# Performance work log

Hardware: AMD Instinct MI355X
Metric: run time of the kernel (lower is better)

## Reference

```python
import math
import jax, jax.numpy as jnp
import numpy as np

B, T, T_P, C, H = 4, 2048, 256, 768, 12
HD = C // H


def setup_inputs() -> dict:
    key = jax.random.key(0)
    k1, k2, k3, k4 = jax.random.split(key, 4)
    x = jax.random.normal(k1, (B, T, C), dtype=jnp.float32)
    prefix = jax.random.normal(k2, (B, T_P, C), dtype=jnp.float32)
    # torch nn.Linear weight layout: (out_features, in_features)
    W_qkv = jax.random.normal(k3, (3 * C, C), dtype=jnp.float32) * (1.0 / math.sqrt(C))
    W_out = jax.random.normal(k4, (C, C), dtype=jnp.float32) * (1.0 / math.sqrt(C))
    return {"x": x, "prefix": prefix, "W_qkv": W_qkv, "W_out": W_out}


def _mac_causal_mask(t_p: int, t: int) -> jnp.ndarray:
    total = t_p + t
    mask = jnp.zeros((total, total), dtype=bool)
    mask = mask.at[:t_p, t_p:].set(True)  # h tokens blocked from x tokens
    causal = jnp.triu(jnp.ones((t, t), dtype=bool), k=1)  # causal within x block
    return mask.at[t_p:, t_p:].set(causal)


def reference(x, prefix, W_qkv, W_out):
    b, t, c = x.shape
    t_p = prefix.shape[1]
    t_all = t_p + t
    x_full = jnp.concatenate([prefix, x], axis=1)          # (B, T_all, C)
    qkv = x_full @ W_qkv.T                                  # (B, T_all, 3C)
    q, k, v = jnp.split(qkv, 3, axis=-1)
    # (B, H, T_all, HD)
    q = q.reshape(b, t_all, H, HD).transpose(0, 2, 1, 3)
    k = k.reshape(b, t_all, H, HD).transpose(0, 2, 1, 3)
    v = v.reshape(b, t_all, H, HD).transpose(0, 2, 1, 3)
    scale = 1.0 / math.sqrt(HD)
    att = jnp.einsum('bhqd,bhkd->bhqk', q, k) * scale       # (B, H, T_all, T_all)
    mask = _mac_causal_mask(t_p, t)
    att = jnp.where(mask[None, None], -jnp.inf, att)
    att = jax.nn.softmax(att, axis=-1)                      # dropout = identity (eval)
    out = jnp.einsum('bhqk,bhkd->bhqd', att, v)             # (B, H, T_all, HD)
    out = out.transpose(0, 2, 1, 3).reshape(b, t_all, c)
    out = out @ W_out.T
    return out[:, t_p:, :]                                  # only x portion (B, T, C)
```

## Files before the change

kernel.cpp:

```cpp
#include <hip/hip_runtime.h>

constexpr int Bn   = 4;
constexpr int Tn   = 2048;
constexpr int TPn  = 256;
constexpr int TALLn = 2304;
constexpr int Cn   = 768;
constexpr int Hn   = 12;
constexpr int HDn  = 64;

typedef __bf16 bf16x4 __attribute__((ext_vector_type(4)));
typedef __bf16 bf16x8 __attribute__((ext_vector_type(8)));
typedef float  f32x4  __attribute__((ext_vector_type(4)));
typedef unsigned u32x4 __attribute__((ext_vector_type(4)));

__device__ __forceinline__ unsigned short f2bf(float f) {
    unsigned int x = __float_as_uint(f);
    x += 0x7fffu + ((x >> 16) & 1u);
    return (unsigned short)(x >> 16);
}

__device__ __forceinline__ unsigned cvt_pk_bf16(float a, float b) {
    unsigned r;
    asm("v_cvt_pk_bf16_f32 %0, %1, %2" : "=v"(r) : "v"(a), "v"(b));
    return r;
}

#define ASYNC16(gsrc, ldst)                                                           \
    __builtin_amdgcn_global_load_lds((__attribute__((address_space(1))) void*)(gsrc), \
                                     (__attribute__((address_space(3))) void*)(ldst), \
                                     16, 0, 0)

__global__ __launch_bounds__(256) void k_build_xfull(
        const float* __restrict__ x, const float* __restrict__ pre,
        unsigned short* __restrict__ xf) {
    int idx = blockIdx.x * 256 + threadIdx.x;
    int row = idx / (Cn / 4);
    int c   = (idx - row * (Cn / 4)) * 4;
    int b = row / TALLn, tt = row - b * TALLn;
    const float* src = (tt < TPn) ? pre + ((size_t)b * TPn + tt) * Cn + c
                                  : x   + ((size_t)b * Tn + (tt - TPn)) * Cn + c;
    float4 f = *reinterpret_cast<const float4*>(src);
    ushort4 o = { f2bf(f.x), f2bf(f.y), f2bf(f.z), f2bf(f.w) };
    *reinterpret_cast<ushort4*>(xf + (size_t)row * Cn + c) = o;
}

__global__ __launch_bounds__(256) void k_cast(
        const float* __restrict__ in, unsigned short* __restrict__ out) {
    int idx = (blockIdx.x * 256 + threadIdx.x) * 4;
    float4 f = *reinterpret_cast<const float4*>(in + idx);
    ushort4 o = { f2bf(f.x), f2bf(f.y), f2bf(f.z), f2bf(f.w) };
    *reinterpret_cast<ushort4*>(out + idx) = o;
}

__global__ __launch_bounds__(256) void k_qkv_gemm(
        const unsigned short* __restrict__ A, const unsigned short* __restrict__ W,
        unsigned short* __restrict__ Qb, unsigned short* __restrict__ Kb,
        unsigned short* __restrict__ Vt) {
    __shared__ __align__(16) unsigned short smem[16384];
    unsigned short* As = smem;
    unsigned short* Bs = smem + 8192;
    const int tid  = threadIdx.x;
    const int wave = tid >> 6;
    const int lane = tid & 63;
    const int g = lane >> 4, l16 = lane & 15;
    const int m0 = blockIdx.x * 128, n0 = blockIdx.y * 128;
    const int wr = wave >> 1, wc = wave & 1;

    f32x4 acc[4][4] = {};

    for (int k0 = 0; k0 < Cn; k0 += 64) {
        #pragma unroll
        for (int inst = 0; inst < 4; ++inst) {
            const int li = inst * 256 + tid;
            const int row = li >> 3, slot = li & 7;
            const int ch = slot ^ (row & 7);
            ASYNC16(A + (size_t)(m0 + row) * Cn + k0 + ch * 8,
                    &As[(inst * 256 + wave * 64) * 8]);
            ASYNC16(W + (size_t)(n0 + row) * Cn + k0 + ch * 8,
                    &Bs[(inst * 256 + wave * 64) * 8]);
        }
        __syncthreads();
        #pragma unroll
        for (int kk = 0; kk < 2; ++kk) {
            bf16x8 af[4], bfv[4];
            #pragma unroll
            for (int mt = 0; mt < 4; ++mt) {
                const int row = wr * 64 + mt * 16 + l16;
                const int slot = (kk * 4 + g) ^ (row & 7);
                af[mt] = *reinterpret_cast<const bf16x8*>(&As[row * 64 + slot * 8]);
            }
            #pragma unroll
            for (int nt = 0; nt < 4; ++nt) {
                const int row = wc * 64 + nt * 16 + l16;
                const int slot = (kk * 4 + g) ^ (row & 7);
                bfv[nt] = *reinterpret_cast<const bf16x8*>(&Bs[row * 64 + slot * 8]);
            }
            #pragma unroll
            for (int mt = 0; mt < 4; ++mt)
                #pragma unroll
                for (int nt = 0; nt < 4; ++nt)
                    acc[mt][nt] = __builtin_amdgcn_mfma_f32_16x16x32_bf16(
                            af[mt], bfv[nt], acc[mt][nt], 0, 0, 0);
        }
        __syncthreads();
    }

    const int b   = m0 / TALLn;
    const int t0  = m0 - b * TALLn;
    const int sel = n0 / Cn;
    const int hn0 = n0 - sel * Cn;
    constexpr float SCQ = 0.18033688011112042f;

    if (sel == 2) {
        #pragma unroll
        for (int mt = 0; mt < 4; ++mt)
            #pragma unroll
            for (int nt = 0; nt < 4; ++nt)
                #pragma unroll
                for (int r = 0; r < 4; ++r) {
                    const int t  = wr * 64 + mt * 16 + g * 4 + r;
                    const int hn = wc * 64 + nt * 16 + l16;
                    smem[hn * 128 + (((t >> 3) ^ (hn & 7)) << 3) + (t & 7)] =
                            f2bf(acc[mt][nt][r]);
                }
        __syncthreads();
        #pragma unroll
        for (int j = 0; j < 8; ++j) {
            const int u  = tid + 256 * j;
            const int hn = u >> 4, tc = u & 15;
            bf16x8 v = *reinterpret_cast<const bf16x8*>(
                    &smem[hn * 128 + ((tc ^ (hn & 7)) << 3)]);
            const int hh = (hn0 + hn) >> 6;
            const int dd = hn & 63;
            *reinterpret_cast<bf16x8*>(
                    &Vt[(((size_t)b * Hn + hh) * HDn + dd) * TALLn + t0 + tc * 8]) = v;
        }
    } else {
        #pragma unroll
        for (int mt = 0; mt < 4; ++mt)
            #pragma unroll
            for (int nt = 0; nt < 4; ++nt)
                #pragma unroll
                for (int r = 0; r < 4; ++r) {
                    const int t  = t0 + wr * 64 + mt * 16 + g * 4 + r;
                    const int hn = hn0 + wc * 64 + nt * 16 + l16;
                    const int h = hn >> 6, d = hn & 63;
                    if (sel == 0)
                        Qb[(((size_t)b * Hn + h) * TALLn + t) * HDn + d] =
                                f2bf(acc[mt][nt][r] * SCQ);
                    else
                        Kb[(((size_t)b * Hn + h) * TALLn + t) * HDn + d] =
                                f2bf(acc[mt][nt][r]);
                }
    }
}

__global__ __launch_bounds__(256) void k_attn(
        const unsigned short* __restrict__ Qb, const unsigned short* __restrict__ Kb,
        const unsigned short* __restrict__ Vt, unsigned short* __restrict__ Ob) {
    __shared__ __align__(16) unsigned short Ks[2][4096];
    __shared__ __align__(16) unsigned short Vs[2][4096];
    const int tid  = threadIdx.x;
    const int wq   = tid >> 6;
    const int lane = tid & 63;
    const int l16  = lane & 15;
    const int g    = lane >> 4;

    const int fb  = blockIdx.x;
    const int j   = fb >> 3;
    const int bh  = 6 * (fb & 7) + (j % 6);
    const int chunk = 31 - (j / 6);
    const int nkt = 5 + chunk;
    const size_t kv = (size_t)bh * TALLn * HDn;

    int koff[4][2];
    #pragma unroll
    for (int band = 0; band < 4; ++band)
        #pragma unroll
        for (int ks = 0; ks < 2; ++ks)
            koff[band][ks] = (band * 16 + l16) * 64 + (((ks * 4 + g) ^ (l16 & 7)) << 3);
    int voffA[2], voffB[2];
    #pragma unroll
    for (int kg = 0; kg < 2; ++kg) {
        voffA[kg] = l16 * 64 + (((4 * kg + (g >> 1)) ^ (l16 & 7)) << 3) + (g & 1) * 4;
        voffB[kg] = l16 * 64 + (((4 * kg + 2 + (g >> 1)) ^ (l16 & 7)) << 3) + (g & 1) * 4;
    }
    const unsigned short* pk[2];
    const unsigned short* pv[2];
    int sdst[2];
    #pragma unroll
    for (int inst = 0; inst < 2; ++inst) {
        const int li = inst * 256 + tid;
        const int row = li >> 3;
        const int ch = (li & 7) ^ (row & 7);
        pk[inst] = Kb + kv + row * HDn + ch * 8;
        pv[inst] = Vt + kv + row * TALLn + ch * 8;
        sdst[inst] = (inst * 256 + wq * 64) * 8;
    }
    constexpr int KSTRIDE = 64 * HDn;
    constexpr int VSTRIDE = 64;

    bf16x8 qf[2];
    {
        const int tq = TPn + chunk * 64 + wq * 16 + l16;
        #pragma unroll
        for (int ks = 0; ks < 2; ++ks)
            qf[ks] = *reinterpret_cast<const bf16x8*>(
                    Qb + kv + (size_t)tq * HDn + ks * 32 + g * 8);
    }

    bf16x8 ones;
    #pragma unroll
    for (int i = 0; i < 8; ++i) ones[i] = (__bf16)1.0f;

    f32x4 oacc[4] = {};
    f32x4 lacc = {};

    #pragma unroll
    for (int inst = 0; inst < 2; ++inst) {
        ASYNC16(pk[inst], &Ks[0][0] + sdst[inst]);
        ASYNC16(pv[inst], &Vs[0][0] + sdst[inst]);
        pk[inst] += KSTRIDE;
        pv[inst] += VSTRIDE;
    }
    __syncthreads();

    int buf = 0;
    for (int t = 0; t < nkt; ++t) {
        if (t + 1 < nkt) {
            #pragma unroll
            for (int inst = 0; inst < 2; ++inst) {
                ASYNC16(pk[inst], &Ks[buf ^ 1][0] + sdst[inst]);
                ASYNC16(pv[inst], &Vs[buf ^ 1][0] + sdst[inst]);
                pk[inst] += KSTRIDE;
                pv[inst] += VSTRIDE;
            }
        }
        const unsigned short* Ksb = &Ks[buf][0];
        const unsigned short* Vsb = &Vs[buf][0];

        f32x4 sacc[4] = {};
        __builtin_amdgcn_s_setprio(1);
        #pragma unroll
        for (int band = 0; band < 4; ++band) {
            bf16x8 k0 = *reinterpret_cast<const bf16x8*>(&Ksb[koff[band][0]]);
            bf16x8 k1 = *reinterpret_cast<const bf16x8*>(&Ksb[koff[band][1]]);
            sacc[band] = __builtin_amdgcn_mfma_f32_16x16x32_bf16(
                    k0, qf[0], sacc[band], 0, 0, 0);
            sacc[band] = __builtin_amdgcn_mfma_f32_16x16x32_bf16(
                    k1, qf[1], sacc[band], 0, 0, 0);
        }
        __builtin_amdgcn_s_setprio(0);

        if (t == nkt - 1) {
            const int lim = TPn + chunk * 64 + wq * 16 + l16 - t * 64;
            #pragma unroll
            for (int band = 0; band < 4; ++band)
                #pragma unroll
                for (int r = 0; r < 4; ++r)
                    sacc[band][r] = (band * 16 + g * 4 + r <= lim) ? sacc[band][r]
                                                                   : -1e30f;
        }
        unsigned dwb[4][2];
        #pragma unroll
        for (int band = 0; band < 4; ++band) {
            const float e0 = exp2f(sacc[band][0]);
            const float e1 = exp2f(sacc[band][1]);
            const float e2 = exp2f(sacc[band][2]);
            const float e3 = exp2f(sacc[band][3]);
            dwb[band][0] = cvt_pk_bf16(e0, e1);
            dwb[band][1] = cvt_pk_bf16(e2, e3);
        }

        __builtin_amdgcn_s_setprio(1);
        #pragma unroll
        for (int kg = 0; kg < 2; ++kg) {
            const u32x4 uu = { dwb[2 * kg][0], dwb[2 * kg][1],
                               dwb[2 * kg + 1][0], dwb[2 * kg + 1][1] };
            const bf16x8 pf = __builtin_bit_cast(bf16x8, uu);
            lacc = __builtin_amdgcn_mfma_f32_16x16x32_bf16(ones, pf, lacc, 0, 0, 0);
            #pragma unroll
            for (int dband = 0; dband < 4; ++dband) {
                bf16x4 a0 = *reinterpret_cast<const bf16x4*>(
                        &Vsb[dband * 1024 + voffA[kg]]);
                bf16x4 a1 = *reinterpret_cast<const bf16x4*>(
                        &Vsb[dband * 1024 + voffB[kg]]);
                bf16x8 vf = __builtin_shufflevector(a0, a1, 0, 1, 2, 3, 4, 5, 6, 7);
                oacc[dband] = __builtin_amdgcn_mfma_f32_16x16x32_bf16(
                        vf, pf, oacc[dband], 0, 0, 0);
            }
        }
        __builtin_amdgcn_s_setprio(0);

        buf ^= 1;
        __syncthreads();
    }

    const int b = bh / Hn, h = bh - b * Hn;
    const float inv = 1.0f / lacc[0];
    const size_t row = (size_t)b * Tn + chunk * 64 + wq * 16 + l16;
    #pragma unroll
    for (int dband = 0; dband < 4; ++dband) {
        ushort4 st;
        st.x = f2bf(oacc[dband][0] * inv);
        st.y = f2bf(oacc[dband][1] * inv);
        st.z = f2bf(oacc[dband][2] * inv);
        st.w = f2bf(oacc[dband][3] * inv);
        *reinterpret_cast<ushort4*>(&Ob[row * Cn + h * 64 + dband * 16 + g * 4]) = st;
    }
}

__global__ __launch_bounds__(256) void k_out_gemm(
        const unsigned short* __restrict__ A, const unsigned short* __restrict__ W,
        float* __restrict__ out) {
    __shared__ __align__(16) unsigned short As[8192];
    __shared__ __align__(16) unsigned short Bs[8192];
    const int tid  = threadIdx.x;
    const int wave = tid >> 6;
    const int lane = tid & 63;
    const int g = lane >> 4, l16 = lane & 15;
    const int m0 = blockIdx.x * 128, n0 = blockIdx.y * 128;
    const int wr = wave >> 1, wc = wave & 1;

    f32x4 acc[4][4] = {};

    for (int k0 = 0; k0 < Cn; k0 += 64) {
        #pragma unroll
        for (int inst = 0; inst < 4; ++inst) {
            const int li = inst * 256 + tid;
            const int row = li >> 3, slot = li & 7;
            const int ch = slot ^ (row & 7);
            ASYNC16(A + (size_t)(m0 + row) * Cn + k0 + ch * 8,
                    &As[(inst * 256 + wave * 64) * 8]);
            ASYNC16(W + (size_t)(n0 + row) * Cn + k0 + ch * 8,
                    &Bs[(inst * 256 + wave * 64) * 8]);
        }
        __syncthreads();
        #pragma unroll
        for (int kk = 0; kk < 2; ++kk) {
            bf16x8 af[4], bfv[4];
            #pragma unroll
            for (int mt = 0; mt < 4; ++mt) {
                const int row = wr * 64 + mt * 16 + l16;
                const int slot = (kk * 4 + g) ^ (row & 7);
                af[mt] = *reinterpret_cast<const bf16x8*>(&As[row * 64 + slot * 8]);
            }
            #pragma unroll
            for (int nt = 0; nt < 4; ++nt) {
                const int row = wc * 64 + nt * 16 + l16;
                const int slot = (kk * 4 + g) ^ (row & 7);
                bfv[nt] = *reinterpret_cast<const bf16x8*>(&Bs[row * 64 + slot * 8]);
            }
            #pragma unroll
            for (int mt = 0; mt < 4; ++mt)
                #pragma unroll
                for (int nt = 0; nt < 4; ++nt)
                    acc[mt][nt] = __builtin_amdgcn_mfma_f32_16x16x32_bf16(
                            af[mt], bfv[nt], acc[mt][nt], 0, 0, 0);
        }
        __syncthreads();
    }

    #pragma unroll
    for (int mt = 0; mt < 4; ++mt)
        #pragma unroll
        for (int nt = 0; nt < 4; ++nt)
            #pragma unroll
            for (int r = 0; r < 4; ++r) {
                const int m = m0 + wr * 64 + mt * 16 + g * 4 + r;
                const int n = n0 + wc * 64 + nt * 16 + l16;
                out[(size_t)m * Cn + n] = acc[mt][nt][r];
            }
}

extern "C" void kernel_launch(void* const* d_in, const int* in_sizes, int n_in,
                              void* d_out, int out_size, void* d_ws, size_t ws_size,
                              hipStream_t stream) {
    const float* x    = (const float*)d_in[0];
    const float* pre  = (const float*)d_in[1];
    const float* wqkv = (const float*)d_in[2];
    const float* wout = (const float*)d_in[3];
    float* out = (float*)d_out;
    char* ws = (char*)d_ws;

    unsigned short* xf  = (unsigned short*)(ws + 0);
    unsigned short* wqb = (unsigned short*)(ws + 14155776);
    unsigned short* wob = (unsigned short*)(ws + 17694720);
    unsigned short* Qb  = (unsigned short*)(ws + 18874368);
    unsigned short* Kb  = (unsigned short*)(ws + 33030144);
    unsigned short* Vt  = (unsigned short*)(ws + 47185920);
    unsigned short* Ob  = (unsigned short*)(ws + 61341696);

    k_build_xfull<<<dim3((Bn * TALLn * Cn / 4) / 256), 256, 0, stream>>>(x, pre, xf);
    k_cast<<<dim3((3 * Cn * Cn / 4) / 256), 256, 0, stream>>>(wqkv, wqb);
    k_cast<<<dim3((Cn * Cn / 4) / 256), 256, 0, stream>>>(wout, wob);
    k_qkv_gemm<<<dim3((Bn * TALLn) / 128, (3 * Cn) / 128), 256, 0, stream>>>(
            xf, wqb, Qb, Kb, Vt);
    k_attn<<<dim3(1536), 256, 0, stream>>>(Qb, Kb, Vt, Ob);
    k_out_gemm<<<dim3((Bn * Tn) / 128, Cn / 128), 256, 0, stream>>>(Ob, wob, out);
}
```

Before: 150.1 us.

## Process two query chunks per attention block with a balanced static schedule

Each attention workgroup now handles 128 query rows (two 64-row chunks) per wave group, so every K/V tile loaded into shared memory is reused by twice as many MFMAs. The grid is halved to 768 blocks and a constant lookup table assigns (head, chunk) pairs so the causal work is balanced across CUs. The cost is doubled accumulator registers, which may reduce occupancy. The first query chunk also runs one extra masked tile.

New measurement: 178.5 us. 1.19x slower.

```diff
diff --git a/kernel.cpp b/kernel.cpp
--- a/kernel.cpp
+++ b/kernel.cpp
@@ -155,6 +155,15 @@
     }
 }
 
+__constant__ unsigned char SCH_CHUNK[96] = {
+     0, 0, 0, 0,15,14,14,13,13,12,12,12,11,11,10, 9,15,15,15,15, 0, 1, 1, 2, 2, 3, 3, 3, 4, 4, 5, 6,
+     7, 8, 9,11, 1, 2, 3, 4, 2, 1, 3, 4,10, 8,10, 8, 8, 7, 6, 4,14,13,12,11,13,14,12,11, 5, 7, 5, 7,
+    15,14,13,11, 6, 6, 5, 5, 7, 9, 7, 6, 1, 3, 2, 5, 0, 1, 2, 4, 9, 9,10,10, 8, 6, 8, 9,14,12,13,10 };
+__constant__ unsigned char SCH_BH[96] = {
+     0, 1, 2, 3, 0, 0, 1, 0, 1, 0, 1, 2, 0, 1, 0, 0, 1, 2, 3, 4, 4, 0, 1, 0, 1, 0, 1, 2, 0, 1, 0, 0,
+     0, 0, 1, 2, 2, 2, 3, 2, 3, 3, 4, 3, 1, 1, 2, 2, 3, 1, 1, 4, 2, 2, 3, 3, 3, 3, 4, 4, 1, 2, 2, 3,
+     5, 4, 4, 5, 2, 3, 3, 4, 4, 2, 5, 4, 4, 5, 4, 5, 5, 5, 5, 5, 3, 4, 3, 4, 4, 5, 5, 5, 5, 5, 5, 5 };
+
 __global__ __launch_bounds__(256) void k_attn(
         const unsigned short* __restrict__ Qb, const unsigned short* __restrict__ Kb,
         const unsigned short* __restrict__ Vt, unsigned short* __restrict__ Ob) {
@@ -168,9 +177,9 @@
 
     const int fb  = blockIdx.x;
     const int j   = fb >> 3;
-    const int bh  = 6 * (fb & 7) + (j % 6);
-    const int chunk = 31 - (j / 6);
-    const int nkt = 5 + chunk;
+    const int bh  = 6 * (fb & 7) + SCH_BH[j];
+    const int chunk = SCH_CHUNK[j];
+    const int nkt = 6 + 2 * chunk;
     const size_t kv = (size_t)bh * TALLn * HDn;
 
     int koff[4][2];
@@ -200,21 +209,24 @@
     constexpr int KSTRIDE = 64 * HDn;
     constexpr int VSTRIDE = 64;
 
-    bf16x8 qf[2];
+    bf16x8 qf0[2], qf1[2];
     {
-        const int tq = TPn + chunk * 64 + wq * 16 + l16;
-        #pragma unroll
-        for (int ks = 0; ks < 2; ++ks)
-            qf[ks] = *reinterpret_cast<const bf16x8*>(
-                    Qb + kv + (size_t)tq * HDn + ks * 32 + g * 8);
+        const int tq0 = TPn + chunk * 128 + wq * 16 + l16;
+        #pragma unroll
+        for (int ks = 0; ks < 2; ++ks) {
+            qf0[ks] = *reinterpret_cast<const bf16x8*>(
+                    Qb + kv + (size_t)tq0 * HDn + ks * 32 + g * 8);
+            qf1[ks] = *reinterpret_cast<const bf16x8*>(
+                    Qb + kv + (size_t)(tq0 + 64) * HDn + ks * 32 + g * 8);
+        }
     }
 
     bf16x8 ones;
     #pragma unroll
     for (int i = 0; i < 8; ++i) ones[i] = (__bf16)1.0f;
 
-    f32x4 oacc[4] = {};
-    f32x4 lacc = {};
+    f32x4 oacc0[4] = {}, oacc1[4] = {};
+    f32x4 lacc0 = {}, lacc1 = {};
 
     #pragma unroll
     for (int inst = 0; inst < 2; ++inst) {
@@ -239,46 +251,51 @@
         const unsigned short* Ksb = &Ks[buf][0];
         const unsigned short* Vsb = &Vs[buf][0];
 
-        f32x4 sacc[4] = {};
+        f32x4 s0[4] = {}, s1[4] = {};
         __builtin_amdgcn_s_setprio(1);
         #pragma unroll
         for (int band = 0; band < 4; ++band) {
             bf16x8 k0 = *reinterpret_cast<const bf16x8*>(&Ksb[koff[band][0]]);
             bf16x8 k1 = *reinterpret_cast<const bf16x8*>(&Ksb[koff[band][1]]);
-            sacc[band] = __builtin_amdgcn_mfma_f32_16x16x32_bf16(
-                    k0, qf[0], sacc[band], 0, 0, 0);
-            sacc[band] = __builtin_amdgcn_mfma_f32_16x16x32_bf16(
-                    k1, qf[1], sacc[band], 0, 0, 0);
+            s0[band] = __builtin_amdgcn_mfma_f32_16x16x32_bf16(k0, qf0[0], s0[band], 0, 0, 0);
+            s0[band] = __builtin_amdgcn_mfma_f32_16x16x32_bf16(k1, qf0[1], s0[band], 0, 0, 0);
+            s1[band] = __builtin_amdgcn_mfma_f32_16x16x32_bf16(k0, qf1[0], s1[band], 0, 0, 0);
+            s1[band] = __builtin_amdgcn_mfma_f32_16x16x32_bf16(k1, qf1[1], s1[band], 0, 0, 0);
         }
         __builtin_amdgcn_s_setprio(0);
 
-        if (t == nkt - 1) {
-            const int lim = TPn + chunk * 64 + wq * 16 + l16 - t * 64;
+        if (t >= nkt - 2) {
+            const int lim = TPn + chunk * 128 + wq * 16 + l16 - t * 64;
             #pragma unroll
             for (int band = 0; band < 4; ++band)
                 #pragma unroll
-                for (int r = 0; r < 4; ++r)
-                    sacc[band][r] = (band * 16 + g * 4 + r <= lim) ? sacc[band][r]
-                                                                   : -1e30f;
-        }
-        unsigned dwb[4][2];
+                for (int r = 0; r < 4; ++r) {
+                    const int key = band * 16 + g * 4 + r;
+                    s0[band][r] = (key <= lim)      ? s0[band][r] : -1e30f;
+                    s1[band][r] = (key <= lim + 64) ? s1[band][r] : -1e30f;
+                }
+        }
+
+        unsigned dw0[4][2], dw1[4][2];
         #pragma unroll
         for (int band = 0; band < 4; ++band) {
-            const float e0 = exp2f(sacc[band][0]);
-            const float e1 = exp2f(sacc[band][1]);
-            const float e2 = exp2f(sacc[band][2]);
-            const float e3 = exp2f(sacc[band][3]);
-            dwb[band][0] = cvt_pk_bf16(e0, e1);
-            dwb[band][1] = cvt_pk_bf16(e2, e3);
+            dw0[band][0] = cvt_pk_bf16(exp2f(s0[band][0]), exp2f(s0[band][1]));
+            dw0[band][1] = cvt_pk_bf16(exp2f(s0[band][2]), exp2f(s0[band][3]));
+            dw1[band][0] = cvt_pk_bf16(exp2f(s1[band][0]), exp2f(s1[band][1]));
+            dw1[band][1] = cvt_pk_bf16(exp2f(s1[band][2]), exp2f(s1[band][3]));
         }
 
         __builtin_amdgcn_s_setprio(1);
         #pragma unroll
         for (int kg = 0; kg < 2; ++kg) {
-            const u32x4 uu = { dwb[2 * kg][0], dwb[2 * kg][1],
-                               dwb[2 * kg + 1][0], dwb[2 * kg + 1][1] };
-            const bf16x8 pf = __builtin_bit_cast(bf16x8, uu);
-            lacc = __builtin_amdgcn_mfma_f32_16x16x32_bf16(ones, pf, lacc, 0, 0, 0);
+            const u32x4 u0 = { dw0[2 * kg][0], dw0[2 * kg][1],
+                               dw0[2 * kg + 1][0], dw0[2 * kg + 1][1] };
+            const u32x4 u1 = { dw1[2 * kg][0], dw1[2 * kg][1],
+                               dw1[2 * kg + 1][0], dw1[2 * kg + 1][1] };
+            const bf16x8 pf0 = __builtin_bit_cast(bf16x8, u0);
+            const bf16x8 pf1 = __builtin_bit_cast(bf16x8, u1);
+            lacc0 = __builtin_amdgcn_mfma_f32_16x16x32_bf16(ones, pf0, lacc0, 0, 0, 0);
+            lacc1 = __builtin_amdgcn_mfma_f32_16x16x32_bf16(ones, pf1, lacc1, 0, 0, 0);
             #pragma unroll
             for (int dband = 0; dband < 4; ++dband) {
                 bf16x4 a0 = *reinterpret_cast<const bf16x4*>(
@@ -286,8 +303,10 @@
                 bf16x4 a1 = *reinterpret_cast<const bf16x4*>(
                         &Vsb[dband * 1024 + voffB[kg]]);
                 bf16x8 vf = __builtin_shufflevector(a0, a1, 0, 1, 2, 3, 4, 5, 6, 7);
-                oacc[dband] = __builtin_amdgcn_mfma_f32_16x16x32_bf16(
-                        vf, pf, oacc[dband], 0, 0, 0);
+                oacc0[dband] = __builtin_amdgcn_mfma_f32_16x16x32_bf16(
+                        vf, pf0, oacc0[dband], 0, 0, 0);
+                oacc1[dband] = __builtin_amdgcn_mfma_f32_16x16x32_bf16(
+                        vf, pf1, oacc1[dband], 0, 0, 0);
             }
         }
         __builtin_amdgcn_s_setprio(0);
@@ -297,16 +316,22 @@
     }
 
     const int b = bh / Hn, h = bh - b * Hn;
-    const float inv = 1.0f / lacc[0];
-    const size_t row = (size_t)b * Tn + chunk * 64 + wq * 16 + l16;
+    const float inv0 = 1.0f / lacc0[0];
+    const float inv1 = 1.0f / lacc1[0];
+    const size_t row0 = (size_t)b * Tn + chunk * 128 + wq * 16 + l16;
     #pragma unroll
     for (int dband = 0; dband < 4; ++dband) {
         ushort4 st;
-        st.x = f2bf(oacc[dband][0] * inv);
-        st.y = f2bf(oacc[dband][1] * inv);
-        st.z = f2bf(oacc[dband][2] * inv);
-        st.w = f2bf(oacc[dband][3] * inv);
-        *reinterpret_cast<ushort4*>(&Ob[row * Cn + h * 64 + dband * 16 + g * 4]) = st;
+        st.x = f2bf(oacc0[dband][0] * inv0);
+        st.y = f2bf(oacc0[dband][1] * inv0);
+        st.z = f2bf(oacc0[dband][2] * inv0);
+        st.w = f2bf(oacc0[dband][3] * inv0);
+        *reinterpret_cast<ushort4*>(&Ob[row0 * Cn + h * 64 + dband * 16 + g * 4]) = st;
+        st.x = f2bf(oacc1[dband][0] * inv1);
+        st.y = f2bf(oacc1[dband][1] * inv1);
+        st.z = f2bf(oacc1[dband][2] * inv1);
+        st.w = f2bf(oacc1[dband][3] * inv1);
+        *reinterpret_cast<ushort4*>(&Ob[(row0 + 64) * Cn + h * 64 + dband * 16 + g * 4]) = st;
     }
 }
 
@@ -396,6 +421,6 @@
     k_cast<<<dim3((Cn * Cn / 4) / 256), 256, 0, stream>>>(wout, wob);
     k_qkv_gemm<<<dim3((Bn * TALLn) / 128, (3 * Cn) / 128), 256, 0, stream>>>(
             xf, wqb, Qb, Kb, Vt);
-    k_attn<<<dim3(1536), 256, 0, stream>>>(Qb, Kb, Vt, Ob);
+    k_attn<<<dim3(768), 256, 0, stream>>>(Qb, Kb, Vt, Ob);
     k_out_gemm<<<dim3((Bn * Tn) / 128, Cn / 128), 256, 0, stream>>>(Ob, wob, out);
 }
```
